# Performance work log

Measured on AMD Instinct MI355X. Metric: run time of the kernel, lower is better.

## Reference

```python
import jax, jax.numpy as jnp
import numpy as np
import math

B, C, IMG_H, IMG_W = 64, 3, 224, 224
P = 14                 # patches per side
PH = PW = 16           # patch size
D = 768                # hidden_d (= C*PH*PW = input_d)
L = 12                 # n_blocks
NH = 12                # n_heads
DH = D // NH           # d_head = 64
FF = 4 * D             # mlp hidden
S = P * P + 1          # 197 tokens (cls + patches)
EXTRACT = (2, 5, 8, 11)
LN_EPS = 1e-5


def _sinusoidal_pos(seq_len, d):
    pos = np.arange(seq_len, dtype=np.float32)[:, None]
    div = np.exp(np.arange(0, d, 2, dtype=np.float32) * -(math.log(10000.0) / d))
    out = np.zeros((seq_len, d), dtype=np.float32)
    out[:, 0::2] = np.sin(pos * div)
    out[:, 1::2] = np.cos(pos * div)
    return jnp.asarray(out)


def setup_inputs() -> dict:
    key = jax.random.key(0)
    ks = jax.random.split(key, 12)
    sc = 0.02
    return {
        "images": jax.random.normal(ks[0], (B, C, IMG_H, IMG_W), jnp.float32),
        "mapper_w": jax.random.normal(ks[1], (D, D), jnp.float32) * sc,  # input_d == D
        "mapper_b": jnp.zeros((D,), jnp.float32),
        "cls_token": jax.random.uniform(ks[2], (1, D), jnp.float32),
        "pos_emb": _sinusoidal_pos(S, D),
        "ln1_g": jnp.ones((L, D), jnp.float32),
        "ln1_b": jnp.zeros((L, D), jnp.float32),
        "qw": jax.random.normal(ks[3], (L, NH, DH, DH), jnp.float32) * sc,
        "qb": jnp.zeros((L, NH, DH), jnp.float32),
        "kw": jax.random.normal(ks[4], (L, NH, DH, DH), jnp.float32) * sc,
        "kb": jnp.zeros((L, NH, DH), jnp.float32),
        "vw": jax.random.normal(ks[5], (L, NH, DH, DH), jnp.float32) * sc,
        "vb": jnp.zeros((L, NH, DH), jnp.float32),
        "ow": jax.random.normal(ks[6], (L, D, D), jnp.float32) * sc,
        "ob": jnp.zeros((L, D), jnp.float32),
        "ln2_g": jnp.ones((L, D), jnp.float32),
        "ln2_b": jnp.zeros((L, D), jnp.float32),
        "mlp_w1": jax.random.normal(ks[7], (L, FF, D), jnp.float32) * sc,
        "mlp_b1": jnp.zeros((L, FF), jnp.float32),
        "mlp_w2": jax.random.normal(ks[8], (L, D, FF), jnp.float32) * sc,
        "mlp_b2": jnp.zeros((L, D), jnp.float32),
    }


def _layernorm(x, g, b):
    mu = jnp.mean(x, axis=-1, keepdims=True)
    var = jnp.mean(jnp.square(x - mu), axis=-1, keepdims=True)
    return (x - mu) * jax.lax.rsqrt(var + LN_EPS) * g + b


def reference(images, mapper_w, mapper_b, cls_token, pos_emb,
              ln1_g, ln1_b, qw, qb, kw, kb, vw, vb, ow, ob,
              ln2_g, ln2_b, mlp_w1, mlp_b1, mlp_w2, mlp_b2):
    n = images.shape[0]
    # patchify: [n,C,H,W] -> [n, P*P, C*PH*PW]
    patches = images.reshape(n, C, P, PH, P, PW)
    patches = patches.transpose(0, 2, 4, 1, 3, 5).reshape(n, P * P, C * PH * PW)
    tokens = patches @ mapper_w.T + mapper_b                      # [n, P*P, D]
    cls = jnp.broadcast_to(cls_token[None], (n, 1, D))
    x = jnp.concatenate([cls, tokens], axis=1) + pos_emb[None]    # [n, S, D]

    extracted = []
    for i in range(L):
        # --- MHSA (note: scale is d_head**2, as in the source) ---
        h = _layernorm(x, ln1_g[i], ln1_b[i])
        hh = h.reshape(n, S, NH, DH)
        q = jnp.einsum('bshd,hed->bshe', hh, qw[i]) + qb[i]
        k = jnp.einsum('bshd,hed->bshe', hh, kw[i]) + kb[i]
        v = jnp.einsum('bshd,hed->bshe', hh, vw[i]) + vb[i]
        scores = jnp.einsum('bqhe,bkhe->bhqk', q, k) / (DH ** 2)
        attn = jax.nn.softmax(scores, axis=-1)
        ctx = jnp.einsum('bhqk,bkhe->bqhe', attn, v).reshape(n, S, D)
        x = x + ctx @ ow[i].T + ob[i]
        # --- MLP ---
        h2 = _layernorm(x, ln2_g[i], ln2_b[i])
        mid = jax.nn.gelu(h2 @ mlp_w1[i].T + mlp_b1[i], approximate=False)
        x = x + mid @ mlp_w2[i].T + mlp_b2[i]
        if i in EXTRACT:
            extracted.append(x)
    return jnp.stack(extracted)  # [4, n, S, D]
```

## Files before the change

kernel.cpp:

```cpp
#include <hip/hip_runtime.h>
#include <hip/hip_bf16.h>
#include <math.h>

static constexpr int NB   = 64;
static constexpr int SS   = 197;
static constexpr int DD   = 768;
static constexpr int NHH  = 12;
static constexpr int DHH  = 64;
static constexpr int FFF  = 3072;
static constexpr int LL   = 12;
static constexpr int TOK  = NB * SS;
static constexpr int NPAT = 196;
static constexpr int PADM = 12672;
static constexpr int PADM2= 12800;
static constexpr long NX  = (long)TOK * DD;

typedef __attribute__((ext_vector_type(8))) short bf16x8;
typedef __attribute__((ext_vector_type(4))) float f32x4;

__device__ inline void gll16(const __hip_bfloat16* g, __hip_bfloat16* l) {
    __builtin_amdgcn_global_load_lds(
        (const __attribute__((address_space(1))) void*)g,
        (__attribute__((address_space(3))) void*)l, 16, 0, 0);
}

template<int EPI, bool OUTBF>
__global__ __launch_bounds__(256, 4) void gemm128(
    const __hip_bfloat16* __restrict__ A, int lda,
    const __hip_bfloat16* __restrict__ Bt, int ldb,
    void* __restrict__ Cout, int ldc,
    const float* __restrict__ bias,
    const float* __restrict__ Rm, int ldr,
    float* __restrict__ out2,
    int M, int N, int K)
{
    __shared__ __hip_bfloat16 sh[3][2][128 * 32];

    const int nbx = gridDim.x;
    const int nwg = nbx * gridDim.y;
    int flat = blockIdx.y * nbx + blockIdx.x;
    {
        int q = nwg >> 3, r = nwg & 7;
        int xcd = flat & 7, idx = flat >> 3;
        flat = (xcd < r ? xcd * (q + 1) : r * (q + 1) + (xcd - r) * q) + idx;
    }
    const int m0 = (flat / nbx) * 128;
    const int n0 = (flat % nbx) * 128;

    const int t = threadIdx.x;
    const int wid = t >> 6, lane = t & 63;
    const int wm = wid >> 1, wn = wid & 1;
    const int l15 = lane & 15, g0 = lane >> 4;
    const int rcol = ((g0 ^ ((l15 >> 1) & 3)) * 8);

    const int srl = t >> 2, sg = t & 3;

    auto stage = [&](int buf, int k0) {
        #pragma unroll
        for (int j = 0; j < 2; ++j) {
            int row = j * 64 + srl;
            int gs = sg ^ ((row >> 1) & 3);
            gll16(A + (long)(m0 + row) * lda + k0 + gs * 8,
                  &sh[buf][0][row * 32 + sg * 8]);
        }
        #pragma unroll
        for (int j = 0; j < 2; ++j) {
            int row = j * 64 + srl;
            int gs = sg ^ ((row >> 1) & 3);
            gll16(Bt + (long)(n0 + row) * ldb + k0 + gs * 8,
                  &sh[buf][1][row * 32 + sg * 8]);
        }
    };

    f32x4 acc[4][4] = {};
    const int NT = K >> 5;

    stage(0, 0);
    stage(1, 32);
    asm volatile("s_waitcnt vmcnt(4)" ::: "memory");
    __builtin_amdgcn_sched_barrier(0);
    __builtin_amdgcn_s_barrier();
    __builtin_amdgcn_sched_barrier(0);

    int cur = 0;
    for (int kt = 0; kt < NT; ++kt) {
        const bool st2 = (kt + 2 < NT);
        const bool w1n = (kt + 1 < NT);
        int stbuf = cur + 2; if (stbuf >= 3) stbuf -= 3;

        bf16x8 af[4], bfr[4];
        #pragma unroll
        for (int mi = 0; mi < 4; ++mi)
            af[mi] = *reinterpret_cast<const bf16x8*>(
                &sh[cur][0][(wm * 64 + mi * 16 + l15) * 32 + rcol]);
        #pragma unroll
        for (int ni = 0; ni < 4; ++ni)
            bfr[ni] = *reinterpret_cast<const bf16x8*>(
                &sh[cur][1][(wn * 64 + ni * 16 + l15) * 32 + rcol]);

        if (st2) stage(stbuf, (kt + 2) << 5);

        asm volatile("s_waitcnt lgkmcnt(0)" ::: "memory");
        __builtin_amdgcn_sched_barrier(0);
        __builtin_amdgcn_s_setprio(1);
        #pragma unroll
        for (int mi = 0; mi < 4; ++mi)
            #pragma unroll
            for (int ni = 0; ni < 4; ++ni)
                acc[mi][ni] = __builtin_amdgcn_mfma_f32_16x16x32_bf16(
                    af[mi], bfr[ni], acc[mi][ni], 0, 0, 0);
        __builtin_amdgcn_s_setprio(0);
        __builtin_amdgcn_sched_barrier(0);
        if (st2)      { asm volatile("s_waitcnt vmcnt(4)" ::: "memory"); }
        else if (w1n) { asm volatile("s_waitcnt vmcnt(0)" ::: "memory"); }
        __builtin_amdgcn_sched_barrier(0);
        __builtin_amdgcn_s_barrier();
        __builtin_amdgcn_sched_barrier(0);

        cur = (cur == 2) ? 0 : cur + 1;
    }

    #pragma unroll
    for (int mi = 0; mi < 4; ++mi) {
        #pragma unroll
        for (int r = 0; r < 4; ++r) {
            int gm = m0 + wm * 64 + mi * 16 + (lane >> 4) * 4 + r;
            if (gm >= M) continue;
            #pragma unroll
            for (int ni = 0; ni < 4; ++ni) {
                int gn = n0 + wn * 64 + ni * 16 + (lane & 15);
                float v = acc[mi][ni][r];
                if (bias) v += bias[gn];
                if (EPI == 1) v += Rm[(long)gm * ldr + gn];
                if (EPI == 2) v = 0.5f * v * (1.0f + erff(v * 0.70710678118654752f));
                if (OUTBF) {
                    ((__hip_bfloat16*)Cout)[(long)gm * ldc + gn] = __float2bfloat16(v);
                } else {
                    ((float*)Cout)[(long)gm * ldc + gn] = v;
                    if (EPI == 1 && out2) out2[(long)gm * ldc + gn] = v;
                }
            }
        }
    }
}

template<int EPI, bool OUTBF>
__global__ __launch_bounds__(512, 4) void gemm256(
    const __hip_bfloat16* __restrict__ A, int lda,
    const __hip_bfloat16* __restrict__ Bt, int ldb,
    void* __restrict__ Cout, int ldc,
    const float* __restrict__ bias,
    const float* __restrict__ Rm, int ldr,
    float* __restrict__ out2,
    int M, int N, int K)
{
    __shared__ __hip_bfloat16 sh[2][(256 + 128) * 32];

    const int nbx = gridDim.x;
    const int nwg = nbx * gridDim.y;
    int flat = blockIdx.y * nbx + blockIdx.x;
    {
        int q = nwg >> 3, r = nwg & 7;
        int xcd = flat & 7, idx = flat >> 3;
        flat = (xcd < r ? xcd * (q + 1) : r * (q + 1) + (xcd - r) * q) + idx;
    }
    const int m0 = (flat / nbx) * 256;
    const int n0 = (flat % nbx) * 128;

    const int t = threadIdx.x;
    const int wid = t >> 6, lane = t & 63;
    const int wm = wid >> 1, wn = wid & 1;
    const int l15 = lane & 15, g0 = lane >> 4;
    const int rcol = ((g0 ^ ((l15 >> 1) & 3)) * 8);

    const int srl = t >> 2, sg = t & 3;

    auto stage = [&](int buf, int k0) {
        #pragma unroll
        for (int j = 0; j < 2; ++j) {
            int row = j * 128 + srl;
            int gs = sg ^ ((row >> 1) & 3);
            gll16(A + (long)(m0 + row) * lda + k0 + gs * 8,
                  &sh[buf][row * 32 + sg * 8]);
        }
        {
            int gs = sg ^ ((srl >> 1) & 3);
            gll16(Bt + (long)(n0 + srl) * ldb + k0 + gs * 8,
                  &sh[buf][8192 + srl * 32 + sg * 8]);
        }
    };

    f32x4 acc[4][4] = {};
    const int NT = K >> 5;

    stage(0, 0);
    stage(1, 32);
    asm volatile("s_waitcnt vmcnt(3)" ::: "memory");
    __builtin_amdgcn_sched_barrier(0);
    __builtin_amdgcn_s_barrier();
    __builtin_amdgcn_sched_barrier(0);

    for (int kt = 0; kt < NT; ++kt) {
        const int cur = kt & 1;
        const bool st2 = (kt + 2 < NT);
        const bool w1n = (kt + 1 < NT);

        bf16x8 af[4], bfr[4];
        #pragma unroll
        for (int mi = 0; mi < 4; ++mi)
            af[mi] = *reinterpret_cast<const bf16x8*>(
                &sh[cur][(wm * 64 + mi * 16 + l15) * 32 + rcol]);
        #pragma unroll
        for (int ni = 0; ni < 4; ++ni)
            bfr[ni] = *reinterpret_cast<const bf16x8*>(
                &sh[cur][8192 + (wn * 64 + ni * 16 + l15) * 32 + rcol]);
        asm volatile("s_waitcnt lgkmcnt(0)" ::: "memory");
        __builtin_amdgcn_sched_barrier(0);
        __builtin_amdgcn_s_barrier();
        __builtin_amdgcn_sched_barrier(0);

        if (st2) stage(cur, (kt + 2) << 5);
        __builtin_amdgcn_s_setprio(1);
        #pragma unroll
        for (int mi = 0; mi < 4; ++mi)
            #pragma unroll
            for (int ni = 0; ni < 4; ++ni)
                acc[mi][ni] = __builtin_amdgcn_mfma_f32_16x16x32_bf16(
                    af[mi], bfr[ni], acc[mi][ni], 0, 0, 0);
        __builtin_amdgcn_s_setprio(0);
        __builtin_amdgcn_sched_barrier(0);
        if (st2)      { asm volatile("s_waitcnt vmcnt(3)" ::: "memory"); }
        else if (w1n) { asm volatile("s_waitcnt vmcnt(0)" ::: "memory"); }
        __builtin_amdgcn_sched_barrier(0);
        __builtin_amdgcn_s_barrier();
        __builtin_amdgcn_sched_barrier(0);
    }

    #pragma unroll
    for (int mi = 0; mi < 4; ++mi) {
        #pragma unroll
        for (int r = 0; r < 4; ++r) {
            int gm = m0 + wm * 64 + mi * 16 + (lane >> 4) * 4 + r;
            if (gm >= M) continue;
            #pragma unroll
            for (int ni = 0; ni < 4; ++ni) {
                int gn = n0 + wn * 64 + ni * 16 + (lane & 15);
                float v = acc[mi][ni][r];
                if (bias) v += bias[gn];
                if (EPI == 1) v += Rm[(long)gm * ldr + gn];
                if (EPI == 2) v = 0.5f * v * (1.0f + erff(v * 0.70710678118654752f));
                if (OUTBF) {
                    ((__hip_bfloat16*)Cout)[(long)gm * ldc + gn] = __float2bfloat16(v);
                } else {
                    ((float*)Cout)[(long)gm * ldc + gn] = v;
                    if (EPI == 1 && out2) out2[(long)gm * ldc + gn] = v;
                }
            }
        }
    }
}

__global__ __launch_bounds__(256) void gemm_qkv(
    const __hip_bfloat16* __restrict__ A, int lda, long sAlo,
    const __hip_bfloat16* __restrict__ Bt, int ldb, long sBhi,
    const float* __restrict__ bias, long sbhi,
    __hip_bfloat16* __restrict__ qb_, __hip_bfloat16* __restrict__ kb_,
    __hip_bfloat16* __restrict__ vb_,
    int M, int N, int K)
{
    __shared__ __hip_bfloat16 As[128 * 64];
    __shared__ __hip_bfloat16 Bs[128 * 64];

    const int zz = blockIdx.z;
    A  += zz * sAlo;
    Bt += zz * sBhi;
    bias += zz * sbhi;

    const int t = threadIdx.x;
    const int wid = t >> 6, lane = t & 63;
    const int wm = wid >> 1, wn = wid & 1;
    const int m0 = blockIdx.y * 128, n0 = blockIdx.x * 128;

    const int srow = t >> 3;
    const int scol = (t & 7) * 8;

    f32x4 acc[4][4] = {};

    for (int k0 = 0; k0 < K; k0 += 64) {
        #pragma unroll
        for (int i = 0; i < 4; ++i) {
            const __hip_bfloat16* ga = A + (long)(m0 + i * 32 + srow) * lda + k0 + scol;
            __hip_bfloat16* la = As + (i * 256 + wid * 64) * 8;
            gll16(ga, la);
            const __hip_bfloat16* gb = Bt + (long)(n0 + i * 32 + srow) * ldb + k0 + scol;
            __hip_bfloat16* lb = Bs + (i * 256 + wid * 64) * 8;
            gll16(gb, lb);
        }
        asm volatile("s_waitcnt vmcnt(0)" ::: "memory");
        __syncthreads();

        #pragma unroll
        for (int kk = 0; kk < 2; ++kk) {
            bf16x8 af[4], bfr[4];
            #pragma unroll
            for (int mi = 0; mi < 4; ++mi)
                af[mi] = *reinterpret_cast<const bf16x8*>(
                    &As[(wm * 64 + mi * 16 + (lane & 15)) * 64 + kk * 32 + (lane >> 4) * 8]);
            #pragma unroll
            for (int ni = 0; ni < 4; ++ni)
                bfr[ni] = *reinterpret_cast<const bf16x8*>(
                    &Bs[(wn * 64 + ni * 16 + (lane & 15)) * 64 + kk * 32 + (lane >> 4) * 8]);
            #pragma unroll
            for (int mi = 0; mi < 4; ++mi)
                #pragma unroll
                for (int ni = 0; ni < 4; ++ni)
                    acc[mi][ni] = __builtin_amdgcn_mfma_f32_16x16x32_bf16(
                        af[mi], bfr[ni], acc[mi][ni], 0, 0, 0);
        }
        __syncthreads();
    }

    #pragma unroll
    for (int mi = 0; mi < 4; ++mi) {
        #pragma unroll
        for (int r = 0; r < 4; ++r) {
            int gm = m0 + wm * 64 + mi * 16 + (lane >> 4) * 4 + r;
            if (gm >= M) continue;
            #pragma unroll
            for (int ni = 0; ni < 4; ++ni) {
                int gn = n0 + wn * 64 + ni * 16 + (lane & 15);
                if (gn >= N) continue;
                float v = acc[mi][ni][r] + bias[gn];
                int c = gn >> 6, e = gn & 63;
                __hip_bfloat16 bv = __float2bfloat16(v);
                __hip_bfloat16* dst = (c == 0) ? qb_ : (c == 1) ? kb_ : vb_;
                dst[(long)gm * DD + zz * 64 + e] = bv;
            }
        }
    }
}

__global__ __launch_bounds__(256) void attn_flash(
    const __hip_bfloat16* __restrict__ qbuf,
    const __hip_bfloat16* __restrict__ kbuf,
    const __hip_bfloat16* __restrict__ vbuf,
    __hip_bfloat16* __restrict__ ctx)
{
    constexpr int KLD = 72;
    constexpr int VLD = 232;
    constexpr int PLD = 232;
    __shared__ __hip_bfloat16 Kl[208 * KLD];
    __shared__ __hip_bfloat16 Vl[64 * VLD];
    __shared__ __hip_bfloat16 Pl[4][16 * PLD];

    const int h = blockIdx.x, b = blockIdx.y;
    const int t = threadIdx.x;
    const int w = t >> 6, lane = t & 63;
    const int l15 = lane & 15, g0 = lane >> 4;

    const long row0 = (long)b * 197;
    const int  hc   = h * 64;

    for (int task = t; task < 208 * 8; task += 256) {
        int r = task >> 3, g = task & 7;
        float4 vv = *reinterpret_cast<const float4*>(kbuf + (row0 + r) * DD + hc + g * 8);
        *reinterpret_cast<float4*>(&Kl[r * KLD + g * 8]) = vv;
    }
    const __hip_bfloat16 bz = __float2bfloat16(0.0f);
    for (int task = t; task < 64 * 27; task += 256) {
        int e = task / 27, c = 197 + (task - e * 27);
        Vl[e * VLD + c] = bz;
    }
    for (int task = t; task < 197 * 8; task += 256) {
        int r = task >> 3, g = task & 7;
        union { float4 f; __hip_bfloat16 hx[8]; } u;
        u.f = *reinterpret_cast<const float4*>(vbuf + (row0 + r) * DD + hc + g * 8);
        #pragma unroll
        for (int j = 0; j < 8; ++j)
            Vl[(g * 8 + j) * VLD + r] = u.hx[j];
    }
    __syncthreads();

    __hip_bfloat16* Pw = Pl[w];

    for (int qc = w; qc < 13; qc += 4) {
        const int q0 = qc * 16;

        const __hip_bfloat16* qsrc = qbuf + (row0 + q0 + l15) * DD + hc + g0 * 8;
        bf16x8 qf0 = *reinterpret_cast<const bf16x8*>(qsrc);
        bf16x8 qf1 = *reinterpret_cast<const bf16x8*>(qsrc + 32);

        f32x4 sacc[13];
        #pragma unroll
        for (int n = 0; n < 13; ++n) {
            bf16x8 kf0 = *reinterpret_cast<const bf16x8*>(&Kl[(n * 16 + l15) * KLD + g0 * 8]);
            bf16x8 kf1 = *reinterpret_cast<const bf16x8*>(&Kl[(n * 16 + l15) * KLD + 32 + g0 * 8]);
            f32x4 z = {0.f, 0.f, 0.f, 0.f};
            z = __builtin_amdgcn_mfma_f32_16x16x32_bf16(qf0, kf0, z, 0, 0, 0);
            sacc[n] = __builtin_amdgcn_mfma_f32_16x16x32_bf16(qf1, kf1, z, 0, 0, 0);
        }

        const int kcol = l15;
        float lrow[4];
        #pragma unroll
        for (int r = 0; r < 4; ++r) {
            float mx = -3.0e38f;
            #pragma unroll
            for (int n = 0; n < 13; ++n) {
                float s = sacc[n][r] * (1.0f / 4096.0f);
                if (n * 16 + kcol < 197) mx = fmaxf(mx, s);
            }
            #pragma unroll
            for (int off = 1; off < 16; off <<= 1) mx = fmaxf(mx, __shfl_xor(mx, off));
            float sum = 0.f;
            #pragma unroll
            for (int n = 0; n < 14; ++n) {
                float p = 0.f;
                if (n < 13 && n * 16 + kcol < 197) {
                    p = __expf(sacc[n][r] * (1.0f / 4096.0f) - mx);
                    sum += p;
                }
                Pw[(g0 * 4 + r) * PLD + n * 16 + kcol] = __float2bfloat16(p);
            }
            #pragma unroll
            for (int off = 1; off < 16; off <<= 1) sum += __shfl_xor(sum, off);
            lrow[r] = sum;
        }

        asm volatile("s_waitcnt lgkmcnt(0)" ::: "memory");

        f32x4 pv[4] = {};
        #pragma unroll
        for (int kc = 0; kc < 7; ++kc) {
            bf16x8 pf = *reinterpret_cast<const bf16x8*>(&Pw[l15 * PLD + kc * 32 + g0 * 8]);
            #pragma unroll
            for (int ni = 0; ni < 4; ++ni) {
                bf16x8 vf = *reinterpret_cast<const bf16x8*>(&Vl[(ni * 16 + l15) * VLD + kc * 32 + g0 * 8]);
                pv[ni] = __builtin_amdgcn_mfma_f32_16x16x32_bf16(pf, vf, pv[ni], 0, 0, 0);
            }
        }

        #pragma unroll
        for (int r = 0; r < 4; ++r) {
            int q = q0 + g0 * 4 + r;
            if (q >= 197) continue;
            float inv = 1.0f / lrow[r];
            #pragma unroll
            for (int ni = 0; ni < 4; ++ni)
                ctx[(row0 + q) * DD + hc + ni * 16 + l15] = __float2bfloat16(pv[ni][r] * inv);
        }
    }
}

__global__ __launch_bounds__(256) void ln_kernel(
    const float* __restrict__ X, const float* __restrict__ g,
    const float* __restrict__ b, __hip_bfloat16* __restrict__ H, int nrows)
{
    int row = blockIdx.x * 4 + (threadIdx.x >> 6);
    if (row >= nrows) return;
    const float* xr = X + (long)row * DD;
    const int lane = threadIdx.x & 63;

    float v[12];
    #pragma unroll
    for (int j = 0; j < 3; ++j) {
        float4 a = *reinterpret_cast<const float4*>(xr + lane * 4 + j * 256);
        v[j * 4 + 0] = a.x; v[j * 4 + 1] = a.y; v[j * 4 + 2] = a.z; v[j * 4 + 3] = a.w;
    }
    float s = 0.f, s2 = 0.f;
    #pragma unroll
    for (int j = 0; j < 12; ++j) { s += v[j]; s2 += v[j] * v[j]; }
    #pragma unroll
    for (int off = 1; off < 64; off <<= 1) {
        s  += __shfl_xor(s,  off);
        s2 += __shfl_xor(s2, off);
    }
    float mu  = s * (1.0f / 768.0f);
    float var = s2 * (1.0f / 768.0f) - mu * mu;
    float rs  = rsqrtf(var + 1e-5f);

    __hip_bfloat16* hr = H + (long)row * DD;
    #pragma unroll
    for (int j = 0; j < 3; ++j) {
        __hip_bfloat16 o[4];
        #pragma unroll
        for (int u = 0; u < 4; ++u) {
            int c = lane * 4 + j * 256 + u;
            o[u] = __float2bfloat16((v[j * 4 + u] - mu) * rs * g[c] + b[c]);
        }
        *reinterpret_cast<uint2*>(hr + lane * 4 + j * 256) = *reinterpret_cast<const uint2*>(o);
    }
}

__global__ void patchify_kernel(const float* __restrict__ img, __hip_bfloat16* __restrict__ patches)
{
    long idx = (long)blockIdx.x * 256 + threadIdx.x;
    const long total = (long)NB * NPAT * DD;
    if (idx >= total) return;
    int k  = (int)(idx % DD);
    long mp = idx / DD;
    int p  = (int)(mp % NPAT);
    long b = mp / NPAT;
    int c = k >> 8;
    int i = (k >> 4) & 15;
    int j = k & 15;
    int pr = p / 14, pc = p % 14;
    int hh = pr * 16 + i, ww = pc * 16 + j;
    patches[idx] = __float2bfloat16(img[((b * 3 + c) * 224 + hh) * 224 + ww]);
}

__global__ void assemble_kernel(const float* __restrict__ tok, const float* __restrict__ cls,
                                const float* __restrict__ pos, float* __restrict__ X)
{
    long idx = (long)blockIdx.x * 256 + threadIdx.x;
    if (idx >= NX) return;
    int d  = (int)(idx % DD);
    long bs = idx / DD;
    int s  = (int)(bs % SS);
    long b = bs / SS;
    float v = (s == 0) ? cls[d] : tok[(b * NPAT + s - 1) * DD + d];
    X[idx] = v + pos[(long)s * DD + d];
}

__global__ void f2b3_kernel(const float* __restrict__ s0, __hip_bfloat16* __restrict__ d0, long c0,
                            const float* __restrict__ s1, __hip_bfloat16* __restrict__ d1, long c1,
                            const float* __restrict__ s2, __hip_bfloat16* __restrict__ d2, long c2)
{
    long i = (long)blockIdx.x * 256 + threadIdx.x;
    const float* s; __hip_bfloat16* d;
    if (i < c0)                { s = s0; d = d0; }
    else if (i < c0 + c1)      { s = s1; d = d1; i -= c0; }
    else if (i < c0 + c1 + c2) { s = s2; d = d2; i -= c0 + c1; }
    else return;
    #pragma unroll
    for (int u = 0; u < 4; ++u) {
        float4 v = *reinterpret_cast<const float4*>(&s[i * 16 + u * 4]);
        __hip_bfloat16 o[4] = { __float2bfloat16(v.x), __float2bfloat16(v.y),
                                __float2bfloat16(v.z), __float2bfloat16(v.w) };
        *reinterpret_cast<uint2*>(&d[i * 16 + u * 4]) = *reinterpret_cast<const uint2*>(o);
    }
}

__global__ void qkvpack_all(const float* __restrict__ qw, const float* __restrict__ kw,
                            const float* __restrict__ vw, const float* __restrict__ qb,
                            const float* __restrict__ kb, const float* __restrict__ vb,
                            __hip_bfloat16* __restrict__ W, float* __restrict__ Bv)
{
    int idx = blockIdx.x * 256 + threadIdx.x;
    if (idx >= LL * NHH * 192 * 64) return;
    int d = idx & 63;
    int rest = idx >> 6;
    int j = rest % 192;
    int lh = rest / 192;
    int c = j >> 6, e = j & 63;
    const float* src = (c == 0 ? qw : c == 1 ? kw : vw) + ((long)lh * 64 + e) * 64 + d;
    W[((long)lh * 256 + j) * 64 + d] = __float2bfloat16(*src);
    if (d == 0) {
        const float* sb = (c == 0 ? qb : c == 1 ? kb : vb) + lh * 64 + e;
        Bv[lh * 192 + j] = *sb;
    }
}

extern "C" void kernel_launch(void* const* d_in, const int* in_sizes, int n_in,
                              void* d_out, int out_size, void* d_ws, size_t ws_size,
                              hipStream_t stream)
{
    const float* images   = (const float*)d_in[0];
    const float* mapper_w = (const float*)d_in[1];
    const float* mapper_b = (const float*)d_in[2];
    const float* cls      = (const float*)d_in[3];
    const float* pos      = (const float*)d_in[4];
    const float* ln1_g    = (const float*)d_in[5];
    const float* ln1_b    = (const float*)d_in[6];
    const float* qw       = (const float*)d_in[7];
    const float* qb       = (const float*)d_in[8];
    const float* kw       = (const float*)d_in[9];
    const float* kb       = (const float*)d_in[10];
    const float* vw       = (const float*)d_in[11];
    const float* vb       = (const float*)d_in[12];
    const float* ow       = (const float*)d_in[13];
    const float* ob       = (const float*)d_in[14];
    const float* ln2_g    = (const float*)d_in[15];
    const float* ln2_b    = (const float*)d_in[16];
    const float* w1       = (const float*)d_in[17];
    const float* b1       = (const float*)d_in[18];
    const float* w2       = (const float*)d_in[19];
    const float* b2       = (const float*)d_in[20];
    float* out = (float*)d_out;

    char* p0 = (char*)d_ws;
    char* pp = p0;
    auto alloc = [&](size_t bytes) { char* r = pp; pp += (bytes + 255) & ~(size_t)255; return r; };

    float*           x       = (float*)          alloc(NX * 4);
    __hip_bfloat16*  h16     = (__hip_bfloat16*) alloc((size_t)PADM2 * DD * 2);
    __hip_bfloat16*  ctx16   = (__hip_bfloat16*) alloc((size_t)PADM * DD * 2);
    __hip_bfloat16*  qbuf    = (__hip_bfloat16*) alloc((size_t)PADM * DD * 2);
    __hip_bfloat16*  kbuf    = (__hip_bfloat16*) alloc((size_t)PADM * DD * 2);
    __hip_bfloat16*  vbuf    = (__hip_bfloat16*) alloc((size_t)PADM * DD * 2);
    __hip_bfloat16*  mw16    = (__hip_bfloat16*) alloc((size_t)DD * DD * 2);
    __hip_bfloat16*  ow16a   = (__hip_bfloat16*) alloc((size_t)LL * DD * DD * 2);
    __hip_bfloat16*  w116a   = (__hip_bfloat16*) alloc((size_t)LL * FFF * DD * 2);
    __hip_bfloat16*  w216a   = (__hip_bfloat16*) alloc((size_t)LL * FFF * DD * 2);
    __hip_bfloat16*  wqkv16a = (__hip_bfloat16*) alloc((size_t)LL * NHH * 256 * 64 * 2);
    float*           bqkva   = (float*)          alloc((size_t)LL * NHH * 192 * 4);
    char*            big     = alloc((size_t)PADM2 * FFF * 2);

    if ((size_t)(pp - p0) > ws_size) return;

    __hip_bfloat16* mid16     = (__hip_bfloat16*)big;
    __hip_bfloat16* patches16 = (__hip_bfloat16*)big;
    float*          tokens    = (float*)(big + (((size_t)NB * NPAT * DD * 2 + 255) & ~(size_t)255));

    {
        const long C0 = (long)LL * DD * DD / 16;
        const long C1 = (long)LL * FFF * DD / 16;
        const long C2 = (long)LL * FFF * DD / 16;
        f2b3_kernel<<<dim3((int)((C0 + C1 + C2 + 255) / 256)), dim3(256), 0, stream>>>(
            ow, ow16a, C0, w1, w116a, C1, w2, w216a, C2);
        f2b3_kernel<<<dim3((int)((DD * DD / 16 + 255) / 256)), dim3(256), 0, stream>>>(
            mapper_w, mw16, DD * DD / 16, nullptr, nullptr, 0, nullptr, nullptr, 0);
        qkvpack_all<<<dim3((LL * NHH * 192 * 64 + 255) / 256), dim3(256), 0, stream>>>(
            qw, kw, vw, qb, kb, vb, wqkv16a, bqkva);
    }

    {
        long n = (long)NB * NPAT * DD;
        patchify_kernel<<<dim3((n + 255) / 256), dim3(256), 0, stream>>>(images, patches16);
        gemm128<0, false><<<dim3(DD / 128, (NB * NPAT) / 128), dim3(256), 0, stream>>>(
            patches16, DD, mw16, DD, tokens, DD, mapper_b, nullptr, 0, nullptr,
            NB * NPAT, DD, DD);
        assemble_kernel<<<dim3((NX + 255) / 256), dim3(256), 0, stream>>>(tokens, cls, pos, x);
    }

    const int MT  = (TOK + 127) / 128;
    const int MT2 = (TOK + 255) / 256;
    const int LNB = (TOK + 3) / 4;

    for (int l = 0; l < 12; ++l) {
        const __hip_bfloat16* ow16 = ow16a + (long)l * DD * DD;
        const __hip_bfloat16* w116 = w116a + (long)l * FFF * DD;
        const __hip_bfloat16* w216 = w216a + (long)l * FFF * DD;
        const __hip_bfloat16* wqkv16 = wqkv16a + (long)l * NHH * 256 * 64;
        const float* bqkv = bqkva + (long)l * NHH * 192;

        ln_kernel<<<dim3(LNB), dim3(256), 0, stream>>>(
            x, ln1_g + l * DD, ln1_b + l * DD, h16, TOK);

        gemm_qkv<<<dim3(2, MT, NHH), dim3(256), 0, stream>>>(
            h16, DD, 64,
            wqkv16, 64, (long)256 * 64,
            bqkv, 192,
            qbuf, kbuf, vbuf,
            TOK, 192, 64);

        attn_flash<<<dim3(NHH, NB), dim3(256), 0, stream>>>(qbuf, kbuf, vbuf, ctx16);

        gemm128<1, false><<<dim3(DD / 128, MT), dim3(256), 0, stream>>>(
            ctx16, DD, ow16, DD, x, DD, ob + l * DD, x, DD, nullptr,
            TOK, DD, DD);

        ln_kernel<<<dim3(LNB), dim3(256), 0, stream>>>(
            x, ln2_g + l * DD, ln2_b + l * DD, h16, TOK);

        gemm256<2, true><<<dim3(FFF / 128, MT2), dim3(512), 0, stream>>>(
            h16, DD, w116, DD, mid16, FFF, b1 + l * FFF, nullptr, 0, nullptr,
            TOK, FFF, DD);

        int slot = (l == 2) ? 0 : (l == 5) ? 1 : (l == 8) ? 2 : (l == 11) ? 3 : -1;
        float* o2 = (slot >= 0) ? out + (long)slot * NX : nullptr;
        gemm256<1, false><<<dim3(DD / 128, MT2), dim3(512), 0, stream>>>(
            mid16, FFF, w216, FFF, x, DD, b2 + l * DD, x, DD, o2,
            TOK, DD, FFF);
    }
}
```

Measured before the change: 5.260 ms.

## Replace gemm128/gemm256 with unified 256x256 eight-wave pipelined GEMM kernel

Replaces both GEMM kernels with a single 256x256-tile, 512-thread kernel that uses BK=64 and an XOR-swizzled LDS layout. The main loop is split into four sub-phases per k-tile, each interleaving global-to-LDS staging with a slice of MFMA work behind barriers. The goal is more data reuse per tile and better overlap of loads with compute. The cost is a larger LDS footprint, fewer resident blocks, and fewer blocks for the N=768 GEMMs (3 column tiles), which risks underfilling the CUs. The ctx16 buffer is enlarged to hold the 256-row padding.

```diff
diff --git a/kernel.cpp b/kernel.cpp
--- a/kernel.cpp
+++ b/kernel.cpp
@@ -24,8 +24,55 @@
         (__attribute__((address_space(3))) void*)l, 16, 0, 0);
 }
 
+#define G8_READ_A(BUF, MI0)                                                   \
+    _Pragma("unroll")                                                         \
+    for (int mm = 0; mm < 2; ++mm) {                                          \
+        _Pragma("unroll")                                                     \
+        for (int kk = 0; kk < 2; ++kk) {                                      \
+            int row = ((MI0) + mm) * 16 + l15;                                \
+            int ph = (kk * 4 + g0) ^ (row & 7);                               \
+            af[mm][kk] = *reinterpret_cast<const bf16x8*>(                    \
+                &sh[BUF][wm][row * 64 + ph * 8]);                             \
+        }                                                                     \
+    }
+
+#define G8_READ_B(BUF)                                                       \
+    _Pragma("unroll")                                                         \
+    for (int ni = 0; ni < 4; ++ni) {                                          \
+        _Pragma("unroll")                                                     \
+        for (int kk = 0; kk < 2; ++kk) {                                      \
+            int row = (wn & 1) * 64 + ni * 16 + l15;                          \
+            int ph = (kk * 4 + g0) ^ (row & 7);                               \
+            bfr[ni][kk] = *reinterpret_cast<const bf16x8*>(                   \
+                &sh[BUF][2 + (wn >> 1)][row * 64 + ph * 8]);                  \
+        }                                                                     \
+    }
+
+#define G8_SYNC_MFMA(MI0)                                                     \
+    __builtin_amdgcn_sched_barrier(0);                                        \
+    __builtin_amdgcn_s_barrier();                                             \
+    asm volatile("s_waitcnt lgkmcnt(0)" ::: "memory");                        \
+    __builtin_amdgcn_sched_barrier(0);                                        \
+    __builtin_amdgcn_s_setprio(1);                                            \
+    _Pragma("unroll")                                                         \
+    for (int mm = 0; mm < 2; ++mm) {                                          \
+        _Pragma("unroll")                                                     \
+        for (int ni = 0; ni < 4; ++ni) {                                      \
+            acc[(MI0) + mm][ni] = __builtin_amdgcn_mfma_f32_16x16x32_bf16(    \
+                af[mm][0], bfr[ni][0], acc[(MI0) + mm][ni], 0, 0, 0);         \
+            acc[(MI0) + mm][ni] = __builtin_amdgcn_mfma_f32_16x16x32_bf16(    \
+                af[mm][1], bfr[ni][1], acc[(MI0) + mm][ni], 0, 0, 0);         \
+        }                                                                     \
+    }                                                                         \
+    __builtin_amdgcn_s_setprio(0);
+
+#define G8_ENDBAR                                                             \
+    __builtin_amdgcn_sched_barrier(0);                                        \
+    __builtin_amdgcn_s_barrier();                                             \
+    __builtin_amdgcn_sched_barrier(0);
+
 template<int EPI, bool OUTBF>
-__global__ __launch_bounds__(256, 4) void gemm128(
+__global__ __launch_bounds__(512, 2) void gemm8p(
     const __hip_bfloat16* __restrict__ A, int lda,
     const __hip_bfloat16* __restrict__ Bt, int ldb,
     void* __restrict__ Cout, int ldc,
@@ -34,7 +81,7 @@
     float* __restrict__ out2,
     int M, int N, int K)
 {
-    __shared__ __hip_bfloat16 sh[3][2][128 * 32];
+    __shared__ __hip_bfloat16 sh[2][4][8192];
 
     const int nbx = gridDim.x;
     const int nwg = nbx * gridDim.y;
@@ -44,207 +91,95 @@
         int xcd = flat & 7, idx = flat >> 3;
         flat = (xcd < r ? xcd * (q + 1) : r * (q + 1) + (xcd - r) * q) + idx;
     }
-    const int m0 = (flat / nbx) * 128;
-    const int n0 = (flat % nbx) * 128;
+    const int m0 = (flat / nbx) * 256;
+    const int n0 = (flat % nbx) * 256;
 
     const int t = threadIdx.x;
     const int wid = t >> 6, lane = t & 63;
-    const int wm = wid >> 1, wn = wid & 1;
+    const int wm = wid >> 2, wn = wid & 3;
     const int l15 = lane & 15, g0 = lane >> 4;
-    const int rcol = ((g0 ^ ((l15 >> 1) & 3)) * 8);
-
-    const int srl = t >> 2, sg = t & 3;
-
-    auto stage = [&](int buf, int k0) {
-        #pragma unroll
-        for (int j = 0; j < 2; ++j) {
-            int row = j * 64 + srl;
-            int gs = sg ^ ((row >> 1) & 3);
-            gll16(A + (long)(m0 + row) * lda + k0 + gs * 8,
-                  &sh[buf][0][row * 32 + sg * 8]);
-        }
-        #pragma unroll
-        for (int j = 0; j < 2; ++j) {
-            int row = j * 64 + srl;
-            int gs = sg ^ ((row >> 1) & 3);
-            gll16(Bt + (long)(n0 + row) * ldb + k0 + gs * 8,
-                  &sh[buf][1][row * 32 + sg * 8]);
+
+    const int u0row = t >> 3, uphys = t & 7;
+    const int u1row = u0row + 64;
+
+    auto stageHalf = [&](int buf, int slot, const __hip_bfloat16* Mp,
+                         int baseRow, int ld, int k0) {
+        {
+            int lsl = uphys ^ (u0row & 7);
+            gll16(Mp + (long)(baseRow + u0row) * ld + k0 + lsl * 8,
+                  &sh[buf][slot][t * 8]);
+        }
+        {
+            int lsl = uphys ^ (u1row & 7);
+            gll16(Mp + (long)(baseRow + u1row) * ld + k0 + lsl * 8,
+                  &sh[buf][slot][(t + 512) * 8]);
         }
     };
 
-    f32x4 acc[4][4] = {};
-    const int NT = K >> 5;
-
-    stage(0, 0);
-    stage(1, 32);
+    f32x4 acc[8][4] = {};
+    bf16x8 af[2][2], bfr[4][2];
+    const int NT = K >> 6;
+    const int ITERS = NT >> 1;
+
+    stageHalf(0, 0, A,  m0,       lda, 0);
+    stageHalf(0, 1, A,  m0 + 128, lda, 0);
+    stageHalf(0, 2, Bt, n0,       ldb, 0);
+    stageHalf(0, 3, Bt, n0 + 128, ldb, 0);
+    stageHalf(1, 2, Bt, n0,       ldb, 64);
+    stageHalf(1, 3, Bt, n0 + 128, ldb, 64);
     asm volatile("s_waitcnt vmcnt(4)" ::: "memory");
     __builtin_amdgcn_sched_barrier(0);
     __builtin_amdgcn_s_barrier();
     __builtin_amdgcn_sched_barrier(0);
 
-    int cur = 0;
-    for (int kt = 0; kt < NT; ++kt) {
-        const bool st2 = (kt + 2 < NT);
-        const bool w1n = (kt + 1 < NT);
-        int stbuf = cur + 2; if (stbuf >= 3) stbuf -= 3;
-
-        bf16x8 af[4], bfr[4];
-        #pragma unroll
-        for (int mi = 0; mi < 4; ++mi)
-            af[mi] = *reinterpret_cast<const bf16x8*>(
-                &sh[cur][0][(wm * 64 + mi * 16 + l15) * 32 + rcol]);
-        #pragma unroll
-        for (int ni = 0; ni < 4; ++ni)
-            bfr[ni] = *reinterpret_cast<const bf16x8*>(
-                &sh[cur][1][(wn * 64 + ni * 16 + l15) * 32 + rcol]);
-
-        if (st2) stage(stbuf, (kt + 2) << 5);
-
-        asm volatile("s_waitcnt lgkmcnt(0)" ::: "memory");
+    for (int it = 0; it < ITERS; ++it) {
+        const bool stn = (it + 1 < ITERS);
+        const int kOdd = (2 * it + 1) << 6;
+        const int kE2  = (2 * it + 2) << 6;
+        const int kO2  = (2 * it + 3) << 6;
+
+        G8_READ_B(0); G8_READ_A(0, 0);
+        stageHalf(1, 0, A, m0, lda, kOdd);
+        G8_SYNC_MFMA(0); G8_ENDBAR;
+        G8_READ_A(0, 2);
+        stageHalf(1, 1, A, m0 + 128, lda, kOdd);
+        G8_SYNC_MFMA(2); G8_ENDBAR;
+        G8_READ_A(0, 4);
+        if (stn) stageHalf(0, 2, Bt, n0, ldb, kE2);
+        G8_SYNC_MFMA(4); G8_ENDBAR;
+        G8_READ_A(0, 6);
+        if (stn) stageHalf(0, 3, Bt, n0 + 128, ldb, kE2);
+        G8_SYNC_MFMA(6);
         __builtin_amdgcn_sched_barrier(0);
-        __builtin_amdgcn_s_setprio(1);
-        #pragma unroll
-        for (int mi = 0; mi < 4; ++mi)
-            #pragma unroll
-            for (int ni = 0; ni < 4; ++ni)
-                acc[mi][ni] = __builtin_amdgcn_mfma_f32_16x16x32_bf16(
-                    af[mi], bfr[ni], acc[mi][ni], 0, 0, 0);
-        __builtin_amdgcn_s_setprio(0);
+        if (stn) { asm volatile("s_waitcnt vmcnt(4)" ::: "memory"); }
+        else     { asm volatile("s_waitcnt vmcnt(0)" ::: "memory"); }
+        G8_ENDBAR;
+        G8_READ_B(1); G8_READ_A(1, 0);
+        if (stn) stageHalf(0, 0, A, m0, lda, kE2);
+        G8_SYNC_MFMA(0); G8_ENDBAR;
+        G8_READ_A(1, 2);
+        if (stn) stageHalf(0, 1, A, m0 + 128, lda, kE2);
+        G8_SYNC_MFMA(2); G8_ENDBAR;
+        G8_READ_A(1, 4);
+        if (stn) stageHalf(1, 2, Bt, n0, ldb, kO2);
+        G8_SYNC_MFMA(4); G8_ENDBAR;
+        G8_READ_A(1, 6);
+        if (stn) stageHalf(1, 3, Bt, n0 + 128, ldb, kO2);
+        G8_SYNC_MFMA(6);
         __builtin_amdgcn_sched_barrier(0);
-        if (st2)      { asm volatile("s_waitcnt vmcnt(4)" ::: "memory"); }
-        else if (w1n) { asm volatile("s_waitcnt vmcnt(0)" ::: "memory"); }
-        __builtin_amdgcn_sched_barrier(0);
-        __builtin_amdgcn_s_barrier();
-        __builtin_amdgcn_sched_barrier(0);
-
-        cur = (cur == 2) ? 0 : cur + 1;
+        if (stn) { asm volatile("s_waitcnt vmcnt(4)" ::: "memory"); }
+        G8_ENDBAR;
     }
 
     #pragma unroll
-    for (int mi = 0; mi < 4; ++mi) {
+    for (int mi = 0; mi < 8; ++mi) {
         #pragma unroll
         for (int r = 0; r < 4; ++r) {
-            int gm = m0 + wm * 64 + mi * 16 + (lane >> 4) * 4 + r;
+            int gm = m0 + wm * 128 + mi * 16 + g0 * 4 + r;
             if (gm >= M) continue;
             #pragma unroll
             for (int ni = 0; ni < 4; ++ni) {
-                int gn = n0 + wn * 64 + ni * 16 + (lane & 15);
-                float v = acc[mi][ni][r];
-                if (bias) v += bias[gn];
-                if (EPI == 1) v += Rm[(long)gm * ldr + gn];
-                if (EPI == 2) v = 0.5f * v * (1.0f + erff(v * 0.70710678118654752f));
-                if (OUTBF) {
-                    ((__hip_bfloat16*)Cout)[(long)gm * ldc + gn] = __float2bfloat16(v);
-                } else {
-                    ((float*)Cout)[(long)gm * ldc + gn] = v;
-                    if (EPI == 1 && out2) out2[(long)gm * ldc + gn] = v;
-                }
-            }
-        }
-    }
-}
-
-template<int EPI, bool OUTBF>
-__global__ __launch_bounds__(512, 4) void gemm256(
-    const __hip_bfloat16* __restrict__ A, int lda,
-    const __hip_bfloat16* __restrict__ Bt, int ldb,
-    void* __restrict__ Cout, int ldc,
-    const float* __restrict__ bias,
-    const float* __restrict__ Rm, int ldr,
-    float* __restrict__ out2,
-    int M, int N, int K)
-{
-    __shared__ __hip_bfloat16 sh[2][(256 + 128) * 32];
-
-    const int nbx = gridDim.x;
-    const int nwg = nbx * gridDim.y;
-    int flat = blockIdx.y * nbx + blockIdx.x;
-    {
-        int q = nwg >> 3, r = nwg & 7;
-        int xcd = flat & 7, idx = flat >> 3;
-        flat = (xcd < r ? xcd * (q + 1) : r * (q + 1) + (xcd - r) * q) + idx;
-    }
-    const int m0 = (flat / nbx) * 256;
-    const int n0 = (flat % nbx) * 128;
-
-    const int t = threadIdx.x;
-    const int wid = t >> 6, lane = t & 63;
-    const int wm = wid >> 1, wn = wid & 1;
-    const int l15 = lane & 15, g0 = lane >> 4;
-    const int rcol = ((g0 ^ ((l15 >> 1) & 3)) * 8);
-
-    const int srl = t >> 2, sg = t & 3;
-
-    auto stage = [&](int buf, int k0) {
-        #pragma unroll
-        for (int j = 0; j < 2; ++j) {
-            int row = j * 128 + srl;
-            int gs = sg ^ ((row >> 1) & 3);
-            gll16(A + (long)(m0 + row) * lda + k0 + gs * 8,
-                  &sh[buf][row * 32 + sg * 8]);
-        }
-        {
-            int gs = sg ^ ((srl >> 1) & 3);
-            gll16(Bt + (long)(n0 + srl) * ldb + k0 + gs * 8,
-                  &sh[buf][8192 + srl * 32 + sg * 8]);
-        }
-    };
-
-    f32x4 acc[4][4] = {};
-    const int NT = K >> 5;
-
-    stage(0, 0);
-    stage(1, 32);
-    asm volatile("s_waitcnt vmcnt(3)" ::: "memory");
-    __builtin_amdgcn_sched_barrier(0);
-    __builtin_amdgcn_s_barrier();
-    __builtin_amdgcn_sched_barrier(0);
-
-    for (int kt = 0; kt < NT; ++kt) {
-        const int cur = kt & 1;
-        const bool st2 = (kt + 2 < NT);
-        const bool w1n = (kt + 1 < NT);
-
-        bf16x8 af[4], bfr[4];
-        #pragma unroll
-        for (int mi = 0; mi < 4; ++mi)
-            af[mi] = *reinterpret_cast<const bf16x8*>(
-                &sh[cur][(wm * 64 + mi * 16 + l15) * 32 + rcol]);
-        #pragma unroll
-        for (int ni = 0; ni < 4; ++ni)
-            bfr[ni] = *reinterpret_cast<const bf16x8*>(
-                &sh[cur][8192 + (wn * 64 + ni * 16 + l15) * 32 + rcol]);
-        asm volatile("s_waitcnt lgkmcnt(0)" ::: "memory");
-        __builtin_amdgcn_sched_barrier(0);
-        __builtin_amdgcn_s_barrier();
-        __builtin_amdgcn_sched_barrier(0);
-
-        if (st2) stage(cur, (kt + 2) << 5);
-        __builtin_amdgcn_s_setprio(1);
-        #pragma unroll
-        for (int mi = 0; mi < 4; ++mi)
-            #pragma unroll
-            for (int ni = 0; ni < 4; ++ni)
-                acc[mi][ni] = __builtin_amdgcn_mfma_f32_16x16x32_bf16(
-                    af[mi], bfr[ni], acc[mi][ni], 0, 0, 0);
-        __builtin_amdgcn_s_setprio(0);
-        __builtin_amdgcn_sched_barrier(0);
-        if (st2)      { asm volatile("s_waitcnt vmcnt(3)" ::: "memory"); }
-        else if (w1n) { asm volatile("s_waitcnt vmcnt(0)" ::: "memory"); }
-        __builtin_amdgcn_sched_barrier(0);
-        __builtin_amdgcn_s_barrier();
-        __builtin_amdgcn_sched_barrier(0);
-    }
-
-    #pragma unroll
-    for (int mi = 0; mi < 4; ++mi) {
-        #pragma unroll
-        for (int r = 0; r < 4; ++r) {
-            int gm = m0 + wm * 64 + mi * 16 + (lane >> 4) * 4 + r;
-            if (gm >= M) continue;
-            #pragma unroll
-            for (int ni = 0; ni < 4; ++ni) {
-                int gn = n0 + wn * 64 + ni * 16 + (lane & 15);
+                int gn = n0 + wn * 64 + ni * 16 + l15;
                 float v = acc[mi][ni][r];
                 if (bias) v += bias[gn];
                 if (EPI == 1) v += Rm[(long)gm * ldr + gn];
@@ -594,7 +529,7 @@
 
     float*           x       = (float*)          alloc(NX * 4);
     __hip_bfloat16*  h16     = (__hip_bfloat16*) alloc((size_t)PADM2 * DD * 2);
-    __hip_bfloat16*  ctx16   = (__hip_bfloat16*) alloc((size_t)PADM * DD * 2);
+    __hip_bfloat16*  ctx16   = (__hip_bfloat16*) alloc((size_t)PADM2 * DD * 2);
     __hip_bfloat16*  qbuf    = (__hip_bfloat16*) alloc((size_t)PADM * DD * 2);
     __hip_bfloat16*  kbuf    = (__hip_bfloat16*) alloc((size_t)PADM * DD * 2);
     __hip_bfloat16*  vbuf    = (__hip_bfloat16*) alloc((size_t)PADM * DD * 2);
@@ -627,14 +562,14 @@
     {
         long n = (long)NB * NPAT * DD;
         patchify_kernel<<<dim3((n + 255) / 256), dim3(256), 0, stream>>>(images, patches16);
-        gemm128<0, false><<<dim3(DD / 128, (NB * NPAT) / 128), dim3(256), 0, stream>>>(
+        gemm8p<0, false><<<dim3(DD / 256, (NB * NPAT) / 256), dim3(512), 0, stream>>>(
             patches16, DD, mw16, DD, tokens, DD, mapper_b, nullptr, 0, nullptr,
             NB * NPAT, DD, DD);
         assemble_kernel<<<dim3((NX + 255) / 256), dim3(256), 0, stream>>>(tokens, cls, pos, x);
     }
 
     const int MT  = (TOK + 127) / 128;
-    const int MT2 = (TOK + 255) / 256;
+    const int MT8 = (TOK + 255) / 256;
     const int LNB = (TOK + 3) / 4;
 
     for (int l = 0; l < 12; ++l) {
@@ -656,20 +591,20 @@
 
         attn_flash<<<dim3(NHH, NB), dim3(256), 0, stream>>>(qbuf, kbuf, vbuf, ctx16);
 
-        gemm128<1, false><<<dim3(DD / 128, MT), dim3(256), 0, stream>>>(
+        gemm8p<1, false><<<dim3(DD / 256, MT8), dim3(512), 0, stream>>>(
             ctx16, DD, ow16, DD, x, DD, ob + l * DD, x, DD, nullptr,
             TOK, DD, DD);
 
         ln_kernel<<<dim3(LNB), dim3(256), 0, stream>>>(
             x, ln2_g + l * DD, ln2_b + l * DD, h16, TOK);
 
-        gemm256<2, true><<<dim3(FFF / 128, MT2), dim3(512), 0, stream>>>(
+        gemm8p<2, true><<<dim3(FFF / 256, MT8), dim3(512), 0, stream>>>(
             h16, DD, w116, DD, mid16, FFF, b1 + l * FFF, nullptr, 0, nullptr,
             TOK, FFF, DD);
 
         int slot = (l == 2) ? 0 : (l == 5) ? 1 : (l == 8) ? 2 : (l == 11) ? 3 : -1;
         float* o2 = (slot >= 0) ? out + (long)slot * NX : nullptr;
-        gemm256<1, false><<<dim3(DD / 128, MT2), dim3(512), 0, stream>>>(
+        gemm8p<1, false><<<dim3(DD / 256, MT8), dim3(512), 0, stream>>>(
             mid16, FFF, w216, FFF, x, DD, b2 + l * DD, x, DD, o2,
             TOK, DD, FFF);
     }
```

Result: slower. 6.329 ms (+20.3%).
